# Optimization experiments

Hardware: AMD Instinct MI355X
Metric: run time of the kernel (lower is better)

## Reference

```python
import jax, jax.numpy as jnp
import numpy as np

NUM_ROIS = 100
FLAT = NUM_ROIS * NUM_ROIS
B = 16
EPS_LN = 1e-5
NEG_SLOPE = 0.2
MASK_NEG = -1e9


def _normal(key, shape, scale):
    return (jax.random.normal(key, shape, dtype=jnp.float32) * scale)


def setup_inputs() -> dict:
    key = jax.random.key(0)
    ks = jax.random.split(key, 32)
    inp = {}
    inp["raw_fc_flat"] = jax.random.normal(ks[0], (B, FLAT), dtype=jnp.float32)
    # graph builder Linear(FLAT, FLAT)
    inp["gb_W"] = _normal(ks[1], (FLAT, FLAT), 1.0 / np.sqrt(FLAT))
    inp["gb_b"] = jnp.zeros((FLAT,), jnp.float32)
    # feature enhancer: Linear(2,8) -> GELU -> Linear(8,16) -> LayerNorm(16)
    inp["fe_W1"] = _normal(ks[2], (2, 8), 1.0 / np.sqrt(2))
    inp["fe_b1"] = jnp.zeros((8,), jnp.float32)
    inp["fe_W2"] = _normal(ks[3], (8, 16), 1.0 / np.sqrt(8))
    inp["fe_b2"] = jnp.zeros((16,), jnp.float32)
    inp["fe_g"] = jnp.ones((16,), jnp.float32)
    inp["fe_beta"] = jnp.zeros((16,), jnp.float32)
    # GATv2 layer 1: in=16, C=128, H=8, concat
    H1, C1 = 8, 128
    inp["Wl1"] = _normal(ks[4], (16, H1 * C1), 1.0 / np.sqrt(16))
    inp["bl1"] = jnp.zeros((H1 * C1,), jnp.float32)
    inp["Wr1"] = _normal(ks[5], (16, H1 * C1), 1.0 / np.sqrt(16))
    inp["br1"] = jnp.zeros((H1 * C1,), jnp.float32)
    inp["att1"] = _normal(ks[6], (H1, C1), 1.0 / np.sqrt(C1))
    inp["bias1"] = jnp.zeros((H1 * C1,), jnp.float32)
    # GATv2 layer 2: in=1024, C=256, H=4, concat
    H2, C2 = 4, 256
    inp["Wl2"] = _normal(ks[7], (1024, H2 * C2), 1.0 / np.sqrt(1024))
    inp["bl2"] = jnp.zeros((H2 * C2,), jnp.float32)
    inp["Wr2"] = _normal(ks[8], (1024, H2 * C2), 1.0 / np.sqrt(1024))
    inp["br2"] = jnp.zeros((H2 * C2,), jnp.float32)
    inp["att2"] = _normal(ks[9], (H2, C2), 1.0 / np.sqrt(C2))
    inp["bias2"] = jnp.zeros((H2 * C2,), jnp.float32)
    # GATv2 layer 3: in=1024, C=128, H=1, concat=False
    H3, C3 = 1, 128
    inp["Wl3"] = _normal(ks[10], (1024, H3 * C3), 1.0 / np.sqrt(1024))
    inp["bl3"] = jnp.zeros((H3 * C3,), jnp.float32)
    inp["Wr3"] = _normal(ks[11], (1024, H3 * C3), 1.0 / np.sqrt(1024))
    inp["br3"] = jnp.zeros((H3 * C3,), jnp.float32)
    inp["att3"] = _normal(ks[12], (H3, C3), 1.0 / np.sqrt(C3))
    inp["bias3"] = jnp.zeros((C3,), jnp.float32)
    return inp


def _gelu(x):
    return jax.nn.gelu(x, approximate=False)


def _gatv2(x, mask, Wl, bl, Wr, br, att, bias, concat):
    # x: [B,N,Fin], mask: [B,N,N] bool, mask[b,i,j] = edge j->i exists (i = target)
    b, n, _ = x.shape
    h, c = att.shape
    xl = (x @ Wl + bl).reshape(b, n, h, c)  # source / message features
    xr = (x @ Wr + br).reshape(b, n, h, c)  # target features
    # GATv2 score: e[b,h,i,j] = att_h . LeakyReLU(xl[b,j,h] + xr[b,i,h])
    g = jax.nn.leaky_relu(xl[:, None, :, :, :] + xr[:, :, None, :, :], NEG_SLOPE)  # [B,i,j,H,C]
    e = jnp.einsum('bijhc,hc->bhij', g, att)
    e = jnp.where(mask[:, None], e, MASK_NEG)
    alpha = jax.nn.softmax(e, axis=-1)
    alpha = jnp.where(mask[:, None], alpha, 0.0)  # zero rows with no neighbors
    out = jnp.einsum('bhij,bjhc->bihc', alpha, xl)  # [B,N,H,C]
    out = out.reshape(b, n, h * c) if concat else out.mean(axis=2)
    return out + bias


def reference(raw_fc_flat, gb_W, gb_b, fe_W1, fe_b1, fe_W2, fe_b2, fe_g, fe_beta,
              Wl1, bl1, Wr1, br1, att1, bias1,
              Wl2, bl2, Wr2, br2, att2, bias2,
              Wl3, bl3, Wr3, br3, att3, bias3):
    bs = raw_fc_flat.shape[0]
    n = NUM_ROIS
    # --- build_graph ---
    adj = jax.nn.sigmoid(raw_fc_flat @ gb_W + gb_b).reshape(bs, n, n)
    adj = (adj + jnp.swapaxes(adj, 1, 2)) * 0.5
    m = adj.mean(axis=2)                 # per-row mean   [B,N]
    s = adj.std(axis=2, ddof=1)          # unbiased std   [B,N]
    b_ft = jnp.stack([m, s + 1e-6], axis=-1)  # [B,N,2]
    hft = _gelu(b_ft @ fe_W1 + fe_b1) @ fe_W2 + fe_b2  # [B,N,16]
    mu = hft.mean(axis=-1, keepdims=True)
    var = hft.var(axis=-1, keepdims=True)
    x = (hft - mu) / jnp.sqrt(var + EPS_LN) * fe_g + fe_beta  # node features [B,N,16]
    thr = jnp.quantile(adj.reshape(bs, -1), 0.75, axis=1)      # per-sample threshold [B]
    mask = adj > thr[:, None, None]  # symmetric edge mask [B,N,N]
    eye = jnp.eye(n, dtype=bool)[None]
    mask_sl = mask | eye  # layers 2,3 add self loops
    # --- GAT stack (eval mode: dropout = identity) ---
    x = _gelu(_gatv2(x, mask, Wl1, bl1, Wr1, br1, att1, bias1, concat=True))
    x = _gelu(_gatv2(x, mask_sl, Wl2, bl2, Wr2, br2, att2, bias2, concat=True))
    x = _gelu(_gatv2(x, mask_sl, Wl3, bl3, Wr3, br3, att3, bias3, concat=False))
    # global mean pool over nodes of each graph
    return x.mean(axis=1)  # [B, gnn_output_dim]
```

## Files before the change

kernel.cpp:

```cpp
#include <hip/hip_runtime.h>
#include <cmath>

#define BATCH 16
#define NROI 100
#define FLATD 10000
#define NTILE 10

typedef __attribute__((ext_vector_type(8))) short s16x8;
typedef __attribute__((ext_vector_type(4))) short s16x4;
typedef __attribute__((ext_vector_type(4))) float f32x4;

__device__ __forceinline__ float sigmoidf(float x) { return 1.0f / (1.0f + expf(-x)); }
__device__ __forceinline__ float geluf(float x) { return 0.5f * x * (1.0f + erff(x * 0.70710678118654752f)); }
__device__ __forceinline__ short f2bf(float x) {
    union { float f; unsigned u; } v; v.f = x;
    unsigned r = v.u + 0x7FFF + ((v.u >> 16) & 1);
    return (short)(r >> 16);
}

__global__ __launch_bounds__(256) void prep_w(const float* __restrict__ Wl2, const float* __restrict__ Wr2,
                                              const float* __restrict__ Wl3, const float* __restrict__ Wr3,
                                              short* __restrict__ Wt2l, short* __restrict__ Wt2r,
                                              short* __restrict__ Wt3l, short* __restrict__ Wt3r) {
    __shared__ float t[32][33];
    int r = blockIdx.x;
    int tid = threadIdx.x;
    const float* in; short* out; int N, xb, yb;
    if (r < 1024)      { in = Wl2; out = Wt2l; N = 1024; xb = r & 31; yb = r >> 5; }
    else if (r < 2048) { r -= 1024; in = Wr2; out = Wt2r; N = 1024; xb = r & 31; yb = r >> 5; }
    else if (r < 2176) { r -= 2048; in = Wl3; out = Wt3l; N = 128;  xb = r & 3;  yb = r >> 2; }
    else               { r -= 2176; in = Wr3; out = Wt3r; N = 128;  xb = r & 3;  yb = r >> 2; }
    int n0 = xb * 32, k0 = yb * 32;
    int tx = tid & 31, ty = tid >> 5;
#pragma unroll
    for (int i = 0; i < 32; i += 8)
        t[ty + i][tx] = in[(size_t)(k0 + ty + i) * N + n0 + tx];
    __syncthreads();
#pragma unroll
    for (int i = 0; i < 32; i += 8)
        out[(size_t)(n0 + ty + i) * 1024 + k0 + tx] = f2bf(t[tx][ty + i]);
}

__global__ __launch_bounds__(256) void gemm1_part(const float* __restrict__ A, const float* __restrict__ W,
                                                  float* __restrict__ part) {
    __shared__ float sA[400][16];
    int ky = blockIdx.y;
    int k0 = ky * 400;
    int tid = threadIdx.x;
    for (int e = tid; e < 16 * 400; e += 256) {
        int m = e / 400, kk = e - m * 400;
        sA[kk][m] = A[(size_t)m * FLATD + k0 + kk];
    }
    __syncthreads();
    int col = blockIdx.x * 512 + tid * 2;
    if (col >= FLATD) return;
    float acc0[16], acc1[16];
#pragma unroll
    for (int m = 0; m < 16; ++m) { acc0[m] = 0.f; acc1[m] = 0.f; }
#pragma unroll 4
    for (int kk = 0; kk < 400; ++kk) {
        float2 w = *reinterpret_cast<const float2*>(W + (size_t)(k0 + kk) * FLATD + col);
        const float* a = sA[kk];
#pragma unroll
        for (int m = 0; m < 16; ++m) { acc0[m] += a[m] * w.x; acc1[m] += a[m] * w.y; }
    }
    float* dst = part + (size_t)ky * 160000;
#pragma unroll
    for (int m = 0; m < 16; ++m) {
        float2 o; o.x = acc0[m]; o.y = acc1[m];
        *reinterpret_cast<float2*>(dst + (size_t)m * FLATD + col) = o;
    }
}

__global__ __launch_bounds__(256) void sym_stats(const float* __restrict__ part, const float* __restrict__ gbb,
                                                 float* __restrict__ adjsym, float* __restrict__ bft) {
    __shared__ float s_adj[50][NROI + 1];
    int b = blockIdx.x;
    int i0 = blockIdx.y * 50;
    for (int idx = threadIdx.x; idx < 50 * NROI; idx += 256) {
        int ii = idx / NROI, j = idx % NROI;
        int i = i0 + ii;
        size_t e1 = (size_t)b * FLATD + i * NROI + j;
        size_t e2 = (size_t)b * FLATD + j * NROI + i;
        float s1 = 0.f, s2 = 0.f;
#pragma unroll
        for (int p = 0; p < 25; ++p) {
            s1 += part[(size_t)p * 160000 + e1];
            s2 += part[(size_t)p * 160000 + e2];
        }
        float v = 0.5f * (sigmoidf(s1 + gbb[i * NROI + j]) + sigmoidf(s2 + gbb[j * NROI + i]));
        s_adj[ii][j] = v;
        adjsym[e1] = v;
    }
    __syncthreads();
    if (threadIdx.x < 50) {
        int i = threadIdx.x;
        float sum = 0.f, sumsq = 0.f;
        for (int j = 0; j < NROI; ++j) { float v = s_adj[i][j]; sum += v; sumsq += v * v; }
        float mean = sum * 0.01f;
        float var = (sumsq - sum * sum * 0.01f) * (1.0f / 99.0f);
        var = fmaxf(var, 0.f);
        bft[(b * NROI + i0 + i) * 2 + 0] = mean;
        bft[(b * NROI + i0 + i) * 2 + 1] = sqrtf(var) + 1e-6f;
    }
}

__global__ __launch_bounds__(512) void quant_enh(const float* __restrict__ adjsym, float* __restrict__ thr,
                                                 const float* __restrict__ bft,
                                                 const float* __restrict__ W1, const float* __restrict__ b1,
                                                 const float* __restrict__ W2, const float* __restrict__ b2,
                                                 const float* __restrict__ g, const float* __restrict__ beta,
                                                 float* __restrict__ x0) {
    if (blockIdx.x >= 16) {
        int idx = (blockIdx.x - 16) * 512 + threadIdx.x;
        if (idx >= BATCH * NROI) return;
        float f0 = bft[idx * 2 + 0], f1 = bft[idx * 2 + 1];
        float h8[8];
#pragma unroll
        for (int u = 0; u < 8; ++u) h8[u] = geluf(W1[u] * f0 + W1[8 + u] * f1 + b1[u]);
        float o[16];
        float mu = 0.f;
#pragma unroll
        for (int v = 0; v < 16; ++v) {
            float t = b2[v];
#pragma unroll
            for (int u = 0; u < 8; ++u) t += h8[u] * W2[u * 16 + v];
            o[v] = t; mu += t;
        }
        mu *= (1.0f / 16.0f);
        float var = 0.f;
#pragma unroll
        for (int v = 0; v < 16; ++v) { float d = o[v] - mu; var += d * d; }
        var *= (1.0f / 16.0f);
        float inv = rsqrtf(var + 1e-5f);
#pragma unroll
        for (int v = 0; v < 16; ++v) x0[idx * 16 + v] = (o[v] - mu) * inv * g[v] + beta[v];
        return;
    }
    __shared__ int red[8];
    __shared__ float redf[8];
    int b = blockIdx.x;
    int tid = threadIdx.x;
    unsigned v[20];
    const unsigned* src = (const unsigned*)(adjsym + (size_t)b * FLATD);
#pragma unroll
    for (int s = 0; s < 20; ++s) {
        int idx = s * 512 + tid;
        v[s] = (idx < FLATD) ? src[idx] : 0x7F800000u;
    }
    int rem = 7499;
    unsigned prefix = 0;
    for (int bit = 30; bit >= 0; --bit) {
        unsigned pshift = prefix >> (bit + 1);
        int c = 0;
#pragma unroll
        for (int s = 0; s < 20; ++s) {
            unsigned x = v[s];
            c += (((x >> (bit + 1)) == pshift) && (((x >> bit) & 1u) == 0u)) ? 1 : 0;
        }
#pragma unroll
        for (int o = 32; o > 0; o >>= 1) c += __shfl_down(c, o, 64);
        if ((tid & 63) == 0) red[tid >> 6] = c;
        __syncthreads();
        int total = red[0] + red[1] + red[2] + red[3] + red[4] + red[5] + red[6] + red[7];
        __syncthreads();
        if (rem >= total) { rem -= total; prefix |= 1u << bit; }
    }
    union { unsigned u; float f; } cv; cv.u = prefix;
    float v0 = cv.f;
    int cle = 0;
    float mg = 3.4e38f;
#pragma unroll
    for (int s = 0; s < 20; ++s) {
        union { unsigned u; float f; } w; w.u = v[s];
        float f = w.f;
        cle += (f <= v0) ? 1 : 0;
        if (f > v0) mg = fminf(mg, f);
    }
#pragma unroll
    for (int o = 32; o > 0; o >>= 1) {
        cle += __shfl_down(cle, o, 64);
        mg = fminf(mg, __shfl_down(mg, o, 64));
    }
    if ((tid & 63) == 0) { red[tid >> 6] = cle; redf[tid >> 6] = mg; }
    __syncthreads();
    if (tid == 0) {
        int tc = 0; float tm = 3.4e38f;
#pragma unroll
        for (int w = 0; w < 8; ++w) { tc += red[w]; tm = fminf(tm, redf[w]); }
        float v1 = (tc >= 7501) ? v0 : tm;
        thr[b] = v0 + 0.25f * (v1 - v0);
    }
}

__global__ __launch_bounds__(256) void proj_gemm(const float* __restrict__ X,
                                                 const float* __restrict__ WL, const float* __restrict__ WR,
                                                 const float* __restrict__ biasL, const float* __restrict__ biasR,
                                                 float* __restrict__ outL, float* __restrict__ outR,
                                                 int K, int Nout) {
    __shared__ float As[16][65];
    __shared__ float Bs[16][128];
    const float* W = blockIdx.z ? WR : WL;
    const float* bias = blockIdx.z ? biasR : biasL;
    float* out = blockIdx.z ? outR : outL;
    int tid = threadIdx.x;
    int tm = tid & 15, tn = tid >> 4;
    int m0 = blockIdx.x * 64, n0 = blockIdx.y * 128;
    float acc[4][8];
#pragma unroll
    for (int r = 0; r < 4; ++r)
#pragma unroll
        for (int c = 0; c < 8; ++c) acc[r][c] = 0.f;
    for (int k0 = 0; k0 < K; k0 += 16) {
        for (int e = tid; e < 64 * 16; e += 256) {
            int kk = e & 15, mm = e >> 4;
            As[kk][mm] = X[(size_t)(m0 + mm) * K + k0 + kk];
        }
        for (int e = tid; e < 16 * 128; e += 256) {
            int nn = e & 127, kk = e >> 7;
            Bs[kk][nn] = W[(size_t)(k0 + kk) * Nout + n0 + nn];
        }
        __syncthreads();
#pragma unroll
        for (int kk = 0; kk < 16; ++kk) {
            float a[4], bb[8];
#pragma unroll
            for (int r = 0; r < 4; ++r) a[r] = As[kk][tm * 4 + r];
#pragma unroll
            for (int c = 0; c < 8; ++c) bb[c] = Bs[kk][tn * 8 + c];
#pragma unroll
            for (int r = 0; r < 4; ++r)
#pragma unroll
                for (int c = 0; c < 8; ++c) acc[r][c] += a[r] * bb[c];
        }
        __syncthreads();
    }
#pragma unroll
    for (int r = 0; r < 4; ++r)
#pragma unroll
        for (int c = 0; c < 8; ++c)
            out[(size_t)(m0 + tm * 4 + r) * Nout + n0 + tn * 8 + c] = acc[r][c] + bias[n0 + tn * 8 + c];
}

__global__ __launch_bounds__(256) void mfma_proj(const short* __restrict__ Xb,
                                                 const short* __restrict__ WtL, const short* __restrict__ WtR,
                                                 const float* __restrict__ biasL, const float* __restrict__ biasR,
                                                 float* __restrict__ outL, float* __restrict__ outR,
                                                 int K, int N) {
    __shared__ short As[64 * 72];
    __shared__ short Bs[64 * 72];
    const short* Wt  = blockIdx.z ? WtR : WtL;
    const float* bias = blockIdx.z ? biasR : biasL;
    float* out = blockIdx.z ? outR : outL;
    int m0 = blockIdx.x * 64, n0 = blockIdx.y * 64;
    int tid = threadIdx.x;
    int row = tid >> 2, part = tid & 3;
    int lane = tid & 63, wave = tid >> 6;
    int wm = wave & 1, wn = wave >> 1;
    int quad = lane >> 4, l16 = lane & 15;
    f32x4 acc00 = {}, acc01 = {}, acc10 = {}, acc11 = {};
    const short* gA = Xb + (size_t)(m0 + row) * K + part * 16;
    const short* gB = Wt + (size_t)(n0 + row) * K + part * 16;
    short* sA = As + row * 72 + part * 16;
    short* sB = Bs + row * 72 + part * 16;
    const short* fA = As + (wm * 32 + l16) * 72 + quad * 8;
    const short* fB = Bs + (wn * 32 + l16) * 72 + quad * 8;
    for (int k0 = 0; k0 < K; k0 += 64) {
        *reinterpret_cast<s16x8*>(sA)     = *reinterpret_cast<const s16x8*>(gA + k0);
        *reinterpret_cast<s16x8*>(sA + 8) = *reinterpret_cast<const s16x8*>(gA + k0 + 8);
        *reinterpret_cast<s16x8*>(sB)     = *reinterpret_cast<const s16x8*>(gB + k0);
        *reinterpret_cast<s16x8*>(sB + 8) = *reinterpret_cast<const s16x8*>(gB + k0 + 8);
        __syncthreads();
#pragma unroll
        for (int ks = 0; ks < 2; ++ks) {
            s16x8 a0 = *reinterpret_cast<const s16x8*>(fA + ks * 32);
            s16x8 a1 = *reinterpret_cast<const s16x8*>(fA + ks * 32 + 16 * 72);
            s16x8 b0 = *reinterpret_cast<const s16x8*>(fB + ks * 32);
            s16x8 b1 = *reinterpret_cast<const s16x8*>(fB + ks * 32 + 16 * 72);
            acc00 = __builtin_amdgcn_mfma_f32_16x16x32_bf16(a0, b0, acc00, 0, 0, 0);
            acc01 = __builtin_amdgcn_mfma_f32_16x16x32_bf16(a0, b1, acc01, 0, 0, 0);
            acc10 = __builtin_amdgcn_mfma_f32_16x16x32_bf16(a1, b0, acc10, 0, 0, 0);
            acc11 = __builtin_amdgcn_mfma_f32_16x16x32_bf16(a1, b1, acc11, 0, 0, 0);
        }
        __syncthreads();
    }
#pragma unroll
    for (int tm = 0; tm < 2; ++tm)
#pragma unroll
        for (int tn = 0; tn < 2; ++tn) {
            const f32x4& a = tm == 0 ? (tn == 0 ? acc00 : acc01) : (tn == 0 ? acc10 : acc11);
            int mbase = m0 + wm * 32 + tm * 16 + quad * 4;
            int n = n0 + wn * 32 + tn * 16 + l16;
            float bv = bias[n];
#pragma unroll
            for (int r = 0; r < 4; ++r)
                out[(size_t)(mbase + r) * N + n] = a[r] + bv;
        }
}

__global__ __launch_bounds__(256) void gat_fused(const float* __restrict__ xl, const float* __restrict__ xr,
                                                 const float* __restrict__ att, const float* __restrict__ adjsym,
                                                 const float* __restrict__ thr, const float* __restrict__ bias,
                                                 short* __restrict__ yout, float* __restrict__ pool_out,
                                                 int H, int C, int self_loop, int pool) {
    __shared__ float s_abs2[2][NTILE][104];
    __shared__ float dl2[2][104];
    __shared__ float p_lds[NTILE][104];
    __shared__ float s_xr[NTILE][256];
    int bh = blockIdx.x;
    int b = bh / H, h = bh % H;
    int i0 = blockIdx.y * NTILE;
    int tid = threadIdx.x;
    const float* atth = att + h * C;

    for (int e = tid; e < NTILE * C; e += 256) {
        int i = e / C, c = e - i * C;
        s_xr[i][c] = xr[((size_t)(b * NROI + i0 + i) * H + h) * C + c];
    }
    __syncthreads();

    {
        int j = tid & 127;
        int cg = tid >> 7;
        int Ch = C >> 1;
        int cbase = cg * Ch;
        const float* xlrow = xl + ((size_t)(b * NROI + (j < NROI ? j : 0)) * H + h) * C + cbase;
        const float* attp0 = atth + cbase;
        float acc[NTILE];
        float dl = 0.f;
#pragma unroll
        for (int i = 0; i < NTILE; ++i) acc[i] = 0.f;
        for (int cc = 0; cc < Ch; cc += 32) {
            float xlr[32];
#pragma unroll
            for (int t = 0; t < 32; t += 4) {
                float4 v = *reinterpret_cast<const float4*>(xlrow + cc + t);
                xlr[t] = v.x; xlr[t + 1] = v.y; xlr[t + 2] = v.z; xlr[t + 3] = v.w;
            }
            const float* attp = attp0 + cc;
#pragma unroll
            for (int t = 0; t < 32; ++t) dl += attp[t] * xlr[t];
#pragma unroll
            for (int i = 0; i < NTILE; ++i) {
                const float* xrp = &s_xr[i][cbase + cc];
                float s = 0.f;
#pragma unroll
                for (int t = 0; t < 32; t += 4) {
                    float4 xv = *reinterpret_cast<const float4*>(xrp + t);
                    s += attp[t + 0] * fabsf(xlr[t + 0] + xv.x);
                    s += attp[t + 1] * fabsf(xlr[t + 1] + xv.y);
                    s += attp[t + 2] * fabsf(xlr[t + 2] + xv.z);
                    s += attp[t + 3] * fabsf(xlr[t + 3] + xv.w);
                }
                acc[i] += s;
            }
        }
        if (j < NROI) {
            dl2[cg][j] = dl;
#pragma unroll
            for (int i = 0; i < NTILE; ++i) s_abs2[cg][i][j] = acc[i];
        }
    }
    __syncthreads();

    if (tid < NTILE * 4) {
        int i = tid >> 2, q = tid & 3;
        int gi = i0 + i;
        int c4 = C >> 2;
        const float* xrrow = xr + ((size_t)(b * NROI + gi) * H + h) * C + q * c4;
        const float* attq = atth + q * c4;
        float dr = 0.f;
        for (int c = 0; c < c4; ++c) dr += attq[c] * xrrow[c];
        dr += __shfl_xor(dr, 1, 64);
        dr += __shfl_xor(dr, 2, 64);
        float tb = thr[b];
        const float* arow = adjsym + (size_t)b * FLATD + gi * NROI + q * 25;
        float em[25];
        float mx = -3.0e38f;
#pragma unroll
        for (int k = 0; k < 25; ++k) {
            int jj = q * 25 + k;
            float e = 0.6f * (dl2[0][jj] + dl2[1][jj] + dr)
                    + 0.4f * (s_abs2[0][i][jj] + s_abs2[1][i][jj]);
            bool edge = (arow[k] > tb) || (self_loop && (jj == gi));
            float v = edge ? e : -1.0e9f;
            em[k] = v;
            mx = fmaxf(mx, v);
        }
        mx = fmaxf(mx, __shfl_xor(mx, 1, 64));
        mx = fmaxf(mx, __shfl_xor(mx, 2, 64));
        float sum = 0.f;
#pragma unroll
        for (int k = 0; k < 25; ++k) {
            em[k] = (em[k] > -0.5e9f) ? expf(em[k] - mx) : 0.f;
            sum += em[k];
        }
        sum += __shfl_xor(sum, 1, 64);
        sum += __shfl_xor(sum, 2, 64);
        float inv = (sum > 0.f) ? 1.0f / sum : 0.f;
#pragma unroll
        for (int k = 0; k < 25; ++k) p_lds[i][q * 25 + k] = em[k] * inv;
    }
    __syncthreads();

    for (int c = tid; c < C; c += 256) {
        float acc[NTILE];
#pragma unroll
        for (int i = 0; i < NTILE; ++i) acc[i] = 0.f;
        const float* xbase = xl + ((size_t)(b * NROI) * H + h) * C + c;
        size_t jstride = (size_t)H * C;
        for (int j0 = 0; j0 < NROI; j0 += 4) {
            float x0v = xbase[(j0 + 0) * jstride];
            float x1v = xbase[(j0 + 1) * jstride];
            float x2v = xbase[(j0 + 2) * jstride];
            float x3v = xbase[(j0 + 3) * jstride];
#pragma unroll
            for (int i = 0; i < NTILE; ++i) {
                float4 p = *reinterpret_cast<const float4*>(&p_lds[i][j0]);
                acc[i] += p.x * x0v + p.y * x1v + p.z * x2v + p.w * x3v;
            }
        }
        float bval = bias[h * C + c];
        if (pool) {
            float pacc = 0.f;
#pragma unroll
            for (int i = 0; i < NTILE; ++i) pacc += 0.01f * geluf(acc[i] + bval);
            atomicAdd(pool_out + b * 128 + c, pacc);
        } else {
#pragma unroll
            for (int i = 0; i < NTILE; ++i) {
                int gi = i0 + i;
                yout[((size_t)(b * NROI + gi) * H + h) * C + c] = f2bf(geluf(acc[i] + bval));
            }
        }
    }
}

extern "C" void kernel_launch(void* const* d_in, const int* in_sizes, int n_in,
                              void* d_out, int out_size, void* d_ws, size_t ws_size,
                              hipStream_t stream) {
    const float* A    = (const float*)d_in[0];
    const float* gbW  = (const float*)d_in[1];
    const float* gbb  = (const float*)d_in[2];
    const float* feW1 = (const float*)d_in[3];
    const float* feb1 = (const float*)d_in[4];
    const float* feW2 = (const float*)d_in[5];
    const float* feb2 = (const float*)d_in[6];
    const float* feg  = (const float*)d_in[7];
    const float* febt = (const float*)d_in[8];
    const float* Wl1  = (const float*)d_in[9];
    const float* bl1  = (const float*)d_in[10];
    const float* Wr1  = (const float*)d_in[11];
    const float* br1  = (const float*)d_in[12];
    const float* att1 = (const float*)d_in[13];
    const float* bias1= (const float*)d_in[14];
    const float* Wl2  = (const float*)d_in[15];
    const float* bl2  = (const float*)d_in[16];
    const float* Wr2  = (const float*)d_in[17];
    const float* br2  = (const float*)d_in[18];
    const float* att2 = (const float*)d_in[19];
    const float* bias2= (const float*)d_in[20];
    const float* Wl3  = (const float*)d_in[21];
    const float* bl3  = (const float*)d_in[22];
    const float* Wr3  = (const float*)d_in[23];
    const float* br3  = (const float*)d_in[24];
    const float* att3 = (const float*)d_in[25];
    const float* bias3= (const float*)d_in[26];

    float* ws = (float*)d_ws;
    float* adj   = ws + 0;
    float* thr   = ws + 160000;
    float* bft   = ws + 160016;
    float* x0    = ws + 163216;
    float* xlbuf = ws + 188816;
    float* xrbuf = ws + 1827216;
    short* Xb    = (short*)(ws + 3465616);
    short* Wt2l  = (short*)(ws + 4284816);
    short* Wt2r  = (short*)(ws + 4809104);
    short* Wt3l  = (short*)(ws + 5333392);
    short* Wt3r  = (short*)(ws + 5398928);
    float* prep  = ws + 5464464;

    hipMemsetAsync(d_out, 0, (size_t)out_size * sizeof(float), stream);

    gemm1_part<<<dim3(20, 25), 256, 0, stream>>>(A, gbW, prep);
    prep_w<<<2304, 256, 0, stream>>>(Wl2, Wr2, Wl3, Wr3, Wt2l, Wt2r, Wt3l, Wt3r);
    sym_stats<<<dim3(BATCH, 2), 256, 0, stream>>>(prep, gbb, adj, bft);
    quant_enh<<<20, 512, 0, stream>>>(adj, thr, bft, feW1, feb1, feW2, feb2, feg, febt, x0);

    proj_gemm<<<dim3(25, 8, 2), 256, 0, stream>>>(x0, Wl1, Wr1, bl1, br1, xlbuf, xrbuf, 16, 1024);
    gat_fused<<<dim3(128, 10), 256, 0, stream>>>(xlbuf, xrbuf, att1, adj, thr, bias1, Xb, nullptr, 8, 128, 0, 0);

    mfma_proj<<<dim3(25, 16, 2), 256, 0, stream>>>(Xb, Wt2l, Wt2r, bl2, br2, xlbuf, xrbuf, 1024, 1024);
    gat_fused<<<dim3(64, 10), 256, 0, stream>>>(xlbuf, xrbuf, att2, adj, thr, bias2, Xb, nullptr, 4, 256, 1, 0);

    mfma_proj<<<dim3(25, 2, 2), 256, 0, stream>>>(Xb, Wt3l, Wt3r, bl3, br3, xlbuf, xrbuf, 1024, 128);
    gat_fused<<<dim3(16, 10), 256, 0, stream>>>(xlbuf, xrbuf, att3, adj, thr, bias3, nullptr, (float*)d_out, 1, 128, 1, 1);
}
```

Before: 940.0 us.

## Fuse front-end kernels: merge GEMM1 with weight prep, and sym/stats/quantile/enhancer

Merges the large graph-builder GEMM and the bf16 weight transpose into one launch, with the weight-prep blocks appended after the GEMM blocks so they can fill idle CUs. The symmetrisation, row statistics, quantile threshold and feature enhancer are combined into a single 1024-thread block per sample that keeps the adjacency in shared memory. This removes the bft buffer and a global round trip of the adjacency. The GEMM inner loop now issues eight weight loads ahead of the FMAs to raise memory-level parallelism. The trade-off is that the fused stage runs only 16 blocks, and the heavier kernel may lose occupancy.

```diff
diff --git a/kernel.cpp b/kernel.cpp
--- a/kernel.cpp
+++ b/kernel.cpp
@@ -18,13 +18,51 @@
     return (short)(r >> 16);
 }
 
-__global__ __launch_bounds__(256) void prep_w(const float* __restrict__ Wl2, const float* __restrict__ Wr2,
-                                              const float* __restrict__ Wl3, const float* __restrict__ Wr3,
-                                              short* __restrict__ Wt2l, short* __restrict__ Wt2r,
-                                              short* __restrict__ Wt3l, short* __restrict__ Wt3r) {
-    __shared__ float t[32][33];
-    int r = blockIdx.x;
+__global__ __launch_bounds__(256) void gemm1_prep(const float* __restrict__ A, const float* __restrict__ W,
+                                                  float* __restrict__ part,
+                                                  const float* __restrict__ Wl2, const float* __restrict__ Wr2,
+                                                  const float* __restrict__ Wl3, const float* __restrict__ Wr3,
+                                                  short* __restrict__ Wt2l, short* __restrict__ Wt2r,
+                                                  short* __restrict__ Wt3l, short* __restrict__ Wt3r) {
+    __shared__ float sA[400][16];
+    int bid = blockIdx.x;
     int tid = threadIdx.x;
+    if (bid < 500) {
+        int bx = bid % 20, ky = bid / 20;
+        int k0 = ky * 400;
+        for (int e = tid; e < 16 * 400; e += 256) {
+            int m = e / 400, kk = e - m * 400;
+            sA[kk][m] = A[(size_t)m * FLATD + k0 + kk];
+        }
+        __syncthreads();
+        int col = bx * 512 + tid * 2;
+        if (col >= FLATD) return;
+        float acc0[16], acc1[16];
+#pragma unroll
+        for (int m = 0; m < 16; ++m) { acc0[m] = 0.f; acc1[m] = 0.f; }
+        const float* wp = W + (size_t)k0 * FLATD + col;
+        for (int kk = 0; kk < 400; kk += 8) {
+            float2 w[8];
+#pragma unroll
+            for (int u = 0; u < 8; ++u)
+                w[u] = *reinterpret_cast<const float2*>(wp + (size_t)(kk + u) * FLATD);
+#pragma unroll
+            for (int u = 0; u < 8; ++u) {
+                const float* a = sA[kk + u];
+#pragma unroll
+                for (int m = 0; m < 16; ++m) { acc0[m] += a[m] * w[u].x; acc1[m] += a[m] * w[u].y; }
+            }
+        }
+        float* dst = part + (size_t)ky * 160000;
+#pragma unroll
+        for (int m = 0; m < 16; ++m) {
+            float2 o; o.x = acc0[m]; o.y = acc1[m];
+            *reinterpret_cast<float2*>(dst + (size_t)m * FLATD + col) = o;
+        }
+        return;
+    }
+    float (*t)[33] = (float(*)[33])&sA[0][0];
+    int r = bid - 500;
     const float* in; short* out; int N, xb, yb;
     if (r < 1024)      { in = Wl2; out = Wt2l; N = 1024; xb = r & 31; yb = r >> 5; }
     else if (r < 2048) { r -= 1024; in = Wr2; out = Wt2r; N = 1024; xb = r & 31; yb = r >> 5; }
@@ -41,137 +79,95 @@
         out[(size_t)(n0 + ty + i) * 1024 + k0 + tx] = f2bf(t[tx][ty + i]);
 }
 
-__global__ __launch_bounds__(256) void gemm1_part(const float* __restrict__ A, const float* __restrict__ W,
-                                                  float* __restrict__ part) {
-    __shared__ float sA[400][16];
-    int ky = blockIdx.y;
-    int k0 = ky * 400;
-    int tid = threadIdx.x;
-    for (int e = tid; e < 16 * 400; e += 256) {
-        int m = e / 400, kk = e - m * 400;
-        sA[kk][m] = A[(size_t)m * FLATD + k0 + kk];
-    }
-    __syncthreads();
-    int col = blockIdx.x * 512 + tid * 2;
-    if (col >= FLATD) return;
-    float acc0[16], acc1[16];
-#pragma unroll
-    for (int m = 0; m < 16; ++m) { acc0[m] = 0.f; acc1[m] = 0.f; }
-#pragma unroll 4
-    for (int kk = 0; kk < 400; ++kk) {
-        float2 w = *reinterpret_cast<const float2*>(W + (size_t)(k0 + kk) * FLATD + col);
-        const float* a = sA[kk];
-#pragma unroll
-        for (int m = 0; m < 16; ++m) { acc0[m] += a[m] * w.x; acc1[m] += a[m] * w.y; }
-    }
-    float* dst = part + (size_t)ky * 160000;
-#pragma unroll
-    for (int m = 0; m < 16; ++m) {
-        float2 o; o.x = acc0[m]; o.y = acc1[m];
-        *reinterpret_cast<float2*>(dst + (size_t)m * FLATD + col) = o;
-    }
-}
-
-__global__ __launch_bounds__(256) void sym_stats(const float* __restrict__ part, const float* __restrict__ gbb,
-                                                 float* __restrict__ adjsym, float* __restrict__ bft) {
-    __shared__ float s_adj[50][NROI + 1];
-    int b = blockIdx.x;
-    int i0 = blockIdx.y * 50;
-    for (int idx = threadIdx.x; idx < 50 * NROI; idx += 256) {
-        int ii = idx / NROI, j = idx % NROI;
-        int i = i0 + ii;
-        size_t e1 = (size_t)b * FLATD + i * NROI + j;
-        size_t e2 = (size_t)b * FLATD + j * NROI + i;
-        float s1 = 0.f, s2 = 0.f;
-#pragma unroll
-        for (int p = 0; p < 25; ++p) {
-            s1 += part[(size_t)p * 160000 + e1];
-            s2 += part[(size_t)p * 160000 + e2];
-        }
-        float v = 0.5f * (sigmoidf(s1 + gbb[i * NROI + j]) + sigmoidf(s2 + gbb[j * NROI + i]));
-        s_adj[ii][j] = v;
-        adjsym[e1] = v;
-    }
-    __syncthreads();
-    if (threadIdx.x < 50) {
-        int i = threadIdx.x;
-        float sum = 0.f, sumsq = 0.f;
-        for (int j = 0; j < NROI; ++j) { float v = s_adj[i][j]; sum += v; sumsq += v * v; }
-        float mean = sum * 0.01f;
-        float var = (sumsq - sum * sum * 0.01f) * (1.0f / 99.0f);
-        var = fmaxf(var, 0.f);
-        bft[(b * NROI + i0 + i) * 2 + 0] = mean;
-        bft[(b * NROI + i0 + i) * 2 + 1] = sqrtf(var) + 1e-6f;
-    }
-}
-
-__global__ __launch_bounds__(512) void quant_enh(const float* __restrict__ adjsym, float* __restrict__ thr,
-                                                 const float* __restrict__ bft,
-                                                 const float* __restrict__ W1, const float* __restrict__ b1,
-                                                 const float* __restrict__ W2, const float* __restrict__ b2,
-                                                 const float* __restrict__ g, const float* __restrict__ beta,
-                                                 float* __restrict__ x0) {
-    if (blockIdx.x >= 16) {
-        int idx = (blockIdx.x - 16) * 512 + threadIdx.x;
-        if (idx >= BATCH * NROI) return;
-        float f0 = bft[idx * 2 + 0], f1 = bft[idx * 2 + 1];
-        float h8[8];
-#pragma unroll
-        for (int u = 0; u < 8; ++u) h8[u] = geluf(W1[u] * f0 + W1[8 + u] * f1 + b1[u]);
-        float o[16];
-        float mu = 0.f;
-#pragma unroll
-        for (int v = 0; v < 16; ++v) {
-            float t = b2[v];
-#pragma unroll
-            for (int u = 0; u < 8; ++u) t += h8[u] * W2[u * 16 + v];
-            o[v] = t; mu += t;
-        }
-        mu *= (1.0f / 16.0f);
-        float var = 0.f;
-#pragma unroll
-        for (int v = 0; v < 16; ++v) { float d = o[v] - mu; var += d * d; }
-        var *= (1.0f / 16.0f);
-        float inv = rsqrtf(var + 1e-5f);
-#pragma unroll
-        for (int v = 0; v < 16; ++v) x0[idx * 16 + v] = (o[v] - mu) * inv * g[v] + beta[v];
-        return;
-    }
-    __shared__ int red[8];
-    __shared__ float redf[8];
+__global__ __launch_bounds__(1024) void sym_quant_enh(const float* __restrict__ part, const float* __restrict__ gbb,
+                                                      float* __restrict__ adjsym, float* __restrict__ thr,
+                                                      const float* __restrict__ W1, const float* __restrict__ b1,
+                                                      const float* __restrict__ W2, const float* __restrict__ b2,
+                                                      const float* __restrict__ g, const float* __restrict__ beta,
+                                                      float* __restrict__ x0) {
+    __shared__ float s_adj[NROI][NROI + 1];
+    __shared__ int redi[16];
+    __shared__ float redf[16];
+    __shared__ float m_l[NROI], s_l[NROI];
     int b = blockIdx.x;
     int tid = threadIdx.x;
-    unsigned v[20];
-    const unsigned* src = (const unsigned*)(adjsym + (size_t)b * FLATD);
-#pragma unroll
-    for (int s = 0; s < 20; ++s) {
-        int idx = s * 512 + tid;
-        v[s] = (idx < FLATD) ? src[idx] : 0x7F800000u;
-    }
+
+    float sig[10];
+#pragma unroll
+    for (int s = 0; s < 10; ++s) {
+        int e = s * 1024 + tid;
+        if (e < FLATD) {
+            const float* pp = part + (size_t)b * FLATD + e;
+            float acc = gbb[e];
+#pragma unroll
+            for (int p = 0; p < 25; ++p) acc += pp[(size_t)p * 160000];
+            sig[s] = sigmoidf(acc);
+            s_adj[e / NROI][e % NROI] = sig[s];
+        }
+    }
+    __syncthreads();
+
+    unsigned v[10];
+#pragma unroll
+    for (int s = 0; s < 10; ++s) {
+        int e = s * 1024 + tid;
+        if (e < FLATD) {
+            int i = e / NROI, j = e - i * NROI;
+            float w = 0.5f * (sig[s] + s_adj[j][i]);
+            union { float f; unsigned u; } cv; cv.f = w;
+            v[s] = cv.u;
+            adjsym[(size_t)b * FLATD + e] = w;
+        } else v[s] = 0x7F800000u;
+    }
+    __syncthreads();
+
+#pragma unroll
+    for (int s = 0; s < 10; ++s) {
+        int e = s * 1024 + tid;
+        if (e < FLATD) {
+            union { unsigned u; float f; } cv; cv.u = v[s];
+            s_adj[e / NROI][e - (e / NROI) * NROI] = cv.f;
+        }
+    }
+    __syncthreads();
+
+    if (tid < NROI) {
+        float sum = 0.f, sumsq = 0.f;
+        for (int j = 0; j < NROI; ++j) { float w = s_adj[tid][j]; sum += w; sumsq += w * w; }
+        float mean = sum * 0.01f;
+        float var = fmaxf((sumsq - sum * sum * 0.01f) * (1.0f / 99.0f), 0.f);
+        m_l[tid] = mean;
+        s_l[tid] = sqrtf(var) + 1e-6f;
+    }
+    __syncthreads();
+
     int rem = 7499;
     unsigned prefix = 0;
     for (int bit = 30; bit >= 0; --bit) {
         unsigned pshift = prefix >> (bit + 1);
         int c = 0;
 #pragma unroll
-        for (int s = 0; s < 20; ++s) {
+        for (int s = 0; s < 10; ++s) {
             unsigned x = v[s];
             c += (((x >> (bit + 1)) == pshift) && (((x >> bit) & 1u) == 0u)) ? 1 : 0;
         }
 #pragma unroll
         for (int o = 32; o > 0; o >>= 1) c += __shfl_down(c, o, 64);
-        if ((tid & 63) == 0) red[tid >> 6] = c;
-        __syncthreads();
-        int total = red[0] + red[1] + red[2] + red[3] + red[4] + red[5] + red[6] + red[7];
+        if ((tid & 63) == 0) redi[tid >> 6] = c;
+        __syncthreads();
+        int total = 0;
+#pragma unroll
+        for (int w = 0; w < 16; ++w) total += redi[w];
         __syncthreads();
         if (rem >= total) { rem -= total; prefix |= 1u << bit; }
     }
-    union { unsigned u; float f; } cv; cv.u = prefix;
-    float v0 = cv.f;
+    union { unsigned u; float f; } cv0; cv0.u = prefix;
+    float v0 = cv0.f;
+
     int cle = 0;
     float mg = 3.4e38f;
 #pragma unroll
-    for (int s = 0; s < 20; ++s) {
+    for (int s = 0; s < 10; ++s) {
         union { unsigned u; float f; } w; w.u = v[s];
         float f = w.f;
         cle += (f <= v0) ? 1 : 0;
@@ -182,14 +178,39 @@
         cle += __shfl_down(cle, o, 64);
         mg = fminf(mg, __shfl_down(mg, o, 64));
     }
-    if ((tid & 63) == 0) { red[tid >> 6] = cle; redf[tid >> 6] = mg; }
+    if ((tid & 63) == 0) { redi[tid >> 6] = cle; redf[tid >> 6] = mg; }
     __syncthreads();
     if (tid == 0) {
         int tc = 0; float tm = 3.4e38f;
 #pragma unroll
-        for (int w = 0; w < 8; ++w) { tc += red[w]; tm = fminf(tm, redf[w]); }
+        for (int w = 0; w < 16; ++w) { tc += redi[w]; tm = fminf(tm, redf[w]); }
         float v1 = (tc >= 7501) ? v0 : tm;
         thr[b] = v0 + 0.25f * (v1 - v0);
+    }
+
+    if (tid < NROI) {
+        float f0 = m_l[tid], f1 = s_l[tid];
+        float h8[8];
+#pragma unroll
+        for (int u = 0; u < 8; ++u) h8[u] = geluf(W1[u] * f0 + W1[8 + u] * f1 + b1[u]);
+        float o[16];
+        float mu = 0.f;
+#pragma unroll
+        for (int vv = 0; vv < 16; ++vv) {
+            float t2 = b2[vv];
+#pragma unroll
+            for (int u = 0; u < 8; ++u) t2 += h8[u] * W2[u * 16 + vv];
+            o[vv] = t2; mu += t2;
+        }
+        mu *= (1.0f / 16.0f);
+        float var = 0.f;
+#pragma unroll
+        for (int vv = 0; vv < 16; ++vv) { float d = o[vv] - mu; var += d * d; }
+        var *= (1.0f / 16.0f);
+        float inv = rsqrtf(var + 1e-5f);
+        int idx = b * NROI + tid;
+#pragma unroll
+        for (int vv = 0; vv < 16; ++vv) x0[idx * 16 + vv] = (o[vv] - mu) * inv * g[vv] + beta[vv];
     }
 }
 
@@ -470,23 +491,21 @@
     float* ws = (float*)d_ws;
     float* adj   = ws + 0;
     float* thr   = ws + 160000;
-    float* bft   = ws + 160016;
-    float* x0    = ws + 163216;
-    float* xlbuf = ws + 188816;
-    float* xrbuf = ws + 1827216;
-    short* Xb    = (short*)(ws + 3465616);
-    short* Wt2l  = (short*)(ws + 4284816);
-    short* Wt2r  = (short*)(ws + 4809104);
-    short* Wt3l  = (short*)(ws + 5333392);
-    short* Wt3r  = (short*)(ws + 5398928);
-    float* prep  = ws + 5464464;
+    float* x0    = ws + 160016;
+    float* xlbuf = ws + 185616;
+    float* xrbuf = ws + 1824016;
+    short* Xb    = (short*)(ws + 3462416);
+    short* Wt2l  = (short*)(ws + 4281616);
+    short* Wt2r  = (short*)(ws + 4805904);
+    short* Wt3l  = (short*)(ws + 5330192);
+    short* Wt3r  = (short*)(ws + 5395728);
+    float* prep  = ws + 5461264;
 
     hipMemsetAsync(d_out, 0, (size_t)out_size * sizeof(float), stream);
 
-    gemm1_part<<<dim3(20, 25), 256, 0, stream>>>(A, gbW, prep);
-    prep_w<<<2304, 256, 0, stream>>>(Wl2, Wr2, Wl3, Wr3, Wt2l, Wt2r, Wt3l, Wt3r);
-    sym_stats<<<dim3(BATCH, 2), 256, 0, stream>>>(prep, gbb, adj, bft);
-    quant_enh<<<20, 512, 0, stream>>>(adj, thr, bft, feW1, feb1, feW2, feb2, feg, febt, x0);
+    gemm1_prep<<<2804, 256, 0, stream>>>(A, gbW, prep, Wl2, Wr2, Wl3, Wr3, Wt2l, Wt2r, Wt3l, Wt3r);
+    sym_quant_enh<<<BATCH, 1024, 0, stream>>>(prep, gbb, adj, thr,
+                                              feW1, feb1, feW2, feb2, feg, febt, x0);
 
     proj_gemm<<<dim3(25, 8, 2), 256, 0, stream>>>(x0, Wl1, Wr1, bl1, br1, xlbuf, xrbuf, 16, 1024);
     gat_fused<<<dim3(128, 10), 256, 0, stream>>>(xlbuf, xrbuf, att1, adj, thr, bias1, Xb, nullptr, 8, 128, 0, 0);
```

Result: faster. 821.9 us (-12.6%).
